# Optimization experiments

Hardware: AMD Instinct MI355X
Metric: run time of the kernel (lower is better)

Reference implementation:

```python
import jax, jax.numpy as jnp
import numpy as np

N_NODES = 20000
N_ATTRS = 5000
IN_FEATURES = 512
OUT_FEATURES = 128
ALPHA = 0.2  # LeakyReLU negative slope
NEG_INF = -9e15


def setup_inputs() -> dict:
    key = jax.random.key(0)
    k1, k2, k3, k4, k5 = jax.random.split(key, 5)
    node_embedding = jax.random.normal(k1, (N_NODES, IN_FEATURES), dtype=jnp.float32)
    attr_embedding = jax.random.normal(k2, (N_ATTRS, IN_FEATURES), dtype=jnp.float32)
    feat_mat = jax.random.randint(k3, (N_NODES, N_ATTRS), 0, 2, dtype=jnp.int32)
    # xavier_uniform with gain=1.414 (as in torch init)
    gain = 1.414
    lim_W = gain * np.sqrt(6.0 / (IN_FEATURES + OUT_FEATURES))
    W = jax.random.uniform(k4, (IN_FEATURES, OUT_FEATURES), minval=-lim_W, maxval=lim_W, dtype=jnp.float32)
    lim_a = gain * np.sqrt(6.0 / (2 * OUT_FEATURES + 1))
    a = jax.random.uniform(k5, (2 * OUT_FEATURES, 1), minval=-lim_a, maxval=lim_a, dtype=jnp.float32)
    return {"node_embedding": node_embedding, "attr_embedding": attr_embedding,
            "feat_mat": feat_mat, "W": W, "a": a}


def reference(node_embedding, attr_embedding, feat_mat, W, a):
    # Linear projections
    node_h = node_embedding @ W            # [N, F]
    attr_h = attr_embedding @ W            # [M, F]
    # Additive attention scores: e[i,j] = leakyrelu(a1.node_h[i] + a2.attr_h[j])
    wh1 = node_h @ a[:OUT_FEATURES, :]     # [N, 1]
    wh2 = attr_h @ a[OUT_FEATURES:, :]     # [M, 1]
    e = jax.nn.leaky_relu(wh1 + wh2.T, negative_slope=ALPHA)  # [N, M]
    # Mask where there is no node-attribute link, then softmax over attrs
    attention = jnp.where(feat_mat > 0, e, NEG_INF)
    attention = jax.nn.softmax(attention, axis=1)
    # (dropout is identity in eval mode)
    h_prime = attention @ attr_h           # [N, F]
    return jax.nn.elu(h_prime)             # concat=True branch
```

## Files before the change

### kernel.cpp

```cpp
#include <hip/hip_runtime.h>

#define N_NODES 20000
#define N_ATTRS 5000
#define IN_F    512
#define OUT_F   128
#define NK      160
#define NSS     80
#define WH2_PAD 5376
#define NEGBIG  -1e30f
#define LOG2E   1.4426950408889634f

typedef _Float16 f16x8 __attribute__((ext_vector_type(8)));
typedef float    f32x4 __attribute__((ext_vector_type(4)));
typedef int      i32x4 __attribute__((ext_vector_type(4)));

__device__ __forceinline__ float fast_exp2(float x) {
    return __builtin_amdgcn_exp2f(x);
}

__device__ __forceinline__ void async16(void* lds_dst, const void* gsrc) {
    __builtin_amdgcn_global_load_lds(
        (const __attribute__((address_space(1))) unsigned int*)gsrc,
        (__attribute__((address_space(3))) unsigned int*)lds_dst, 16, 0, 0);
}

__global__ __launch_bounds__(256) void prep_kernel(
    const float* __restrict__ W, const float* __restrict__ a,
    float* __restrict__ Wa1, float* __restrict__ Wa2, _Float16* __restrict__ Wp) {
    int gt = blockIdx.x * blockDim.x + threadIdx.x;
    if (gt < IN_F) {
        int k = gt;
        float s1 = 0.f, s2 = 0.f;
        for (int f = 0; f < OUT_F; ++f) {
            float w = W[k * OUT_F + f];
            s1 += w * a[f];
            s2 += w * a[OUT_F + f];
        }
        Wa1[k] = s1 * LOG2E;
        Wa2[k] = s2 * LOG2E;
    }
    for (int idx = gt; idx < IN_F * OUT_F; idx += gridDim.x * blockDim.x) {
        int j    = idx & 7;
        int lane = (idx >> 3) & 63;
        int nb   = (idx >> 9) & 7;
        int kb   = idx >> 12;
        int k = kb * 32 + (lane >> 4) * 8 + j;
        int n = nb * 16 + (lane & 15);
        Wp[idx] = (_Float16)W[k * OUT_F + n];
    }
}

__global__ __launch_bounds__(256) void wh_kernel(
    const float* __restrict__ node_emb, const float* __restrict__ attr_emb,
    const float* __restrict__ Wa1, const float* __restrict__ Wa2,
    float* __restrict__ wh1, float* __restrict__ wh2) {
    int wave = threadIdx.x >> 6, lane = threadIdx.x & 63;
    int r = blockIdx.x * 4 + wave;
    const float* src;
    const float* vec;
    float* dst;
    if (r < N_NODES) {
        src = node_emb + (size_t)r * IN_F; vec = Wa1; dst = wh1 + r;
    } else {
        int r2 = r - N_NODES;
        src = attr_emb + (size_t)r2 * IN_F; vec = Wa2; dst = wh2 + r2;
    }
    float4 ra = *reinterpret_cast<const float4*>(src + lane * 8);
    float4 rb = *reinterpret_cast<const float4*>(src + lane * 8 + 4);
    const float* vp = vec + lane * 8;
    float s = ra.x * vp[0] + ra.y * vp[1] + ra.z * vp[2] + ra.w * vp[3]
            + rb.x * vp[4] + rb.y * vp[5] + rb.z * vp[6] + rb.w * vp[7];
#pragma unroll
    for (int off = 1; off < 64; off <<= 1) s += __shfl_xor(s, off, 64);
    if (lane == 0) *dst = s;
}

__global__ __launch_bounds__(256) void max_kernel(
    float* __restrict__ wh2, float* __restrict__ maxp) {
    __shared__ float red[4];
    int t = threadIdx.x;
    float m = -1e30f;
    for (int j = t; j < N_ATTRS; j += 256) m = fmaxf(m, wh2[j]);
    for (int j = N_ATTRS + t; j < WH2_PAD; j += 256) wh2[j] = NEGBIG;
#pragma unroll
    for (int off = 1; off < 64; off <<= 1) m = fmaxf(m, __shfl_xor(m, off, 64));
    int wave = t >> 6, lane = t & 63;
    if (lane == 0) red[wave] = m;
    __syncthreads();
    if (t == 0) *maxp = fmaxf(fmaxf(red[0], red[1]), fmaxf(red[2], red[3]));
}

__global__ __launch_bounds__(64) void attr_h_kernel(
    const float* __restrict__ attr_emb, const _Float16* __restrict__ Wp,
    _Float16* __restrict__ Vp) {
    int lane = threadIdx.x & 63;
    int m = lane & 15, quad = lane >> 4;
    int j0 = blockIdx.x * 16;
    int j = j0 + m;
    bool valid = j < N_ATTRS;
    f32x4 acc[8];
#pragma unroll
    for (int nb = 0; nb < 8; ++nb)
#pragma unroll
        for (int t = 0; t < 4; ++t) acc[nb][t] = 0.f;
    const float* arow = attr_emb + (size_t)j * IN_F;
    for (int kk = 0; kk < IN_F / 32; ++kk) {
        f16x8 afrag;
        if (valid) {
            float4 ra = *reinterpret_cast<const float4*>(arow + kk * 32 + quad * 8);
            float4 rb = *reinterpret_cast<const float4*>(arow + kk * 32 + quad * 8 + 4);
            afrag[0] = (_Float16)ra.x; afrag[1] = (_Float16)ra.y;
            afrag[2] = (_Float16)ra.z; afrag[3] = (_Float16)ra.w;
            afrag[4] = (_Float16)rb.x; afrag[5] = (_Float16)rb.y;
            afrag[6] = (_Float16)rb.z; afrag[7] = (_Float16)rb.w;
        } else {
#pragma unroll
            for (int t = 0; t < 8; ++t) afrag[t] = (_Float16)0.f;
        }
        const _Float16* wbase = Wp + (size_t)(kk * 8) * 64 * 8;
#pragma unroll
        for (int nb = 0; nb < 8; ++nb) {
            f16x8 bfrag;
            __builtin_memcpy(&bfrag, wbase + (nb * 64 + lane) * 8, 16);
            acc[nb] = __builtin_amdgcn_mfma_f32_16x16x32_f16(afrag, bfrag, acc[nb], 0, 0, 0);
        }
    }
#pragma unroll
    for (int nb = 0; nb < 8; ++nb) {
#pragma unroll
        for (int reg = 0; reg < 4; ++reg) {
            int jr = j0 + quad * 4 + reg;
            int n = nb * 16 + m;
            float v = (jr < N_ATTRS) ? acc[nb][reg] : 0.f;
            size_t idx = ((size_t)((jr >> 5) * 8 + nb) * 64 +
                          (((jr >> 3) & 3) * 16 + m)) * 8 + (jr & 7);
            Vp[idx] = (_Float16)v;
        }
    }
}

__global__ __launch_bounds__(256) void pack_kernel(
    const int* __restrict__ feat, unsigned* __restrict__ fmask) {
    int u = blockIdx.x * 256 + threadIdx.x;
    int row = u / 160;
    int kk  = u - row * 160;
    int ko  = (kk & ~31) | ((kk & 31) ^ ((2 * (row & 15)) & 31));
    unsigned bits = 0;
    if (ko < 156) {
        const int* p = feat + (size_t)row * N_ATTRS + ko * 32;
#pragma unroll
        for (int q = 0; q < 8; ++q) {
            i32x4 v = *reinterpret_cast<const i32x4*>(p + q * 4);
            unsigned b = (v.x > 0 ? 1u : 0u) | (v.y > 0 ? 2u : 0u)
                       | (v.z > 0 ? 4u : 0u) | (v.w > 0 ? 8u : 0u);
            bits |= b << (q * 4);
        }
    } else if (ko == 156) {
        const int* p = feat + (size_t)row * N_ATTRS + 4992;
#pragma unroll
        for (int q = 0; q < 2; ++q) {
            i32x4 v = *reinterpret_cast<const i32x4*>(p + q * 4);
            unsigned b = (v.x > 0 ? 1u : 0u) | (v.y > 0 ? 2u : 0u)
                       | (v.z > 0 ? 4u : 0u) | (v.w > 0 ? 8u : 0u);
            bits |= b << (q * 4);
        }
    }
    fmask[u] = bits;
}

__global__ __launch_bounds__(256, 2) void attn_kernel(
    const unsigned* __restrict__ fmask, const float* __restrict__ wh1,
    const float* __restrict__ wh2, const float* __restrict__ maxwh2,
    const _Float16* __restrict__ Vp, float* __restrict__ out) {
    __shared__ __align__(16) char lds[20480];
    __shared__ float rsums[32];

    int wave = threadIdx.x >> 6, lane = threadIdx.x & 63;
    int m = lane & 15, quad = lane >> 4;
    int i0 = blockIdx.x * 32;
    int rg = (wave >> 1) * 16;
    int half = wave & 1;

    {
        const char* src = (const char*)(fmask + (size_t)i0 * 160);
#pragma unroll
        for (int q = 0; q < 5; ++q) {
            int off = q * 4096 + wave * 1024;
            async16(lds + off, src + off + lane * 16);
        }
    }

    float wh1i = wh1[i0 + rg + m];
    float emax = wh1i + maxwh2[0];
    float Mi = fmaxf(emax, 0.2f * emax) - 12.f;

    f32x4 acc[8];
#pragma unroll
    for (int nb = 0; nb < 8; ++nb)
#pragma unroll
        for (int t = 0; t < 4; ++t) acc[nb][t] = 0.f;
    float s = 0.f;

    const unsigned* fml = (const unsigned*)lds;
    int swz = (2 * m) & 31;
    int fbase = (rg + m) * 160;

    f16x8  bf0[8], bf1[8];
    float4 w0a, w0b, w1a, w1b;
    auto loadV = [&](int ss, f16x8* bf, float4& wa, float4& wb) {
        const _Float16* vb = Vp + (size_t)(2 * ss + half) * 4096 + lane * 8;
#pragma unroll
        for (int nb = 0; nb < 8; ++nb)
            bf[nb] = *reinterpret_cast<const f16x8*>(vb + nb * 512);
        const float* wp = wh2 + ss * 64 + half * 32 + quad * 8;
        wa = *reinterpret_cast<const float4*>(wp);
        wb = *reinterpret_cast<const float4*>(wp + 4);
    };

    auto compute = [&](int ss, const f16x8* bf, float4 wa, float4 wb) {
        int k = 2 * ss + half;
        int kk = (k & ~31) | ((k & 31) ^ swz);
        unsigned fm = fml[fbase + kk] >> (quad * 8);
        float wv[8] = {wa.x, wa.y, wa.z, wa.w, wb.x, wb.y, wb.z, wb.w};
        f16x8 afrag;
#pragma unroll
        for (int t = 0; t < 8; ++t) {
            float e = wh1i + wv[t];
            float l = fmaxf(e, 0.2f * e);
            float p = fast_exp2(l - Mi);
            p = (fm & (1u << t)) ? p : 0.f;
            _Float16 ph = (_Float16)p;
            s += (float)ph;
            afrag[t] = ph;
        }
#pragma unroll
        for (int nb = 0; nb < 8; ++nb)
            acc[nb] = __builtin_amdgcn_mfma_f32_16x16x32_f16(afrag, bf[nb], acc[nb], 0, 0, 0);
    };

    loadV(0, bf0, w0a, w0b);
    __syncthreads();

    for (int ss = 0; ss < NSS; ss += 2) {
        loadV(ss + 1, bf1, w1a, w1b);
        compute(ss, bf0, w0a, w0b);
        int kn = (ss + 2 < NSS) ? ss + 2 : NSS - 1;
        loadV(kn, bf0, w0a, w0b);
        compute(ss + 1, bf1, w1a, w1b);
    }

    s += __shfl_xor(s, 16, 64);
    s += __shfl_xor(s, 32, 64);

    __syncthreads();

    float* accp = (float*)lds;
    if (half == 0) {
#pragma unroll
        for (int nb = 0; nb < 8; ++nb)
#pragma unroll
            for (int reg = 0; reg < 4; ++reg)
                accp[(rg + quad * 4 + reg) * 128 + nb * 16 + m] = acc[nb][reg];
        if (lane < 16) rsums[rg + lane] = s;
    }
    __syncthreads();
    if (half == 1) {
#pragma unroll
        for (int nb = 0; nb < 8; ++nb)
#pragma unroll
            for (int reg = 0; reg < 4; ++reg)
                accp[(rg + quad * 4 + reg) * 128 + nb * 16 + m] += acc[nb][reg];
        if (lane < 16) rsums[rg + lane] += s;
    }
    __syncthreads();

    for (int o = threadIdx.x; o < 32 * 128; o += 256) {
        int lr = o >> 7, n = o & 127;
        float v = accp[lr * 128 + n];
        float rs = rsums[lr];
        rs = (rs > 0.f) ? rs : 1.f;
        float h = v / rs;
        float ov = (h > 0.f) ? h : (fast_exp2(h * LOG2E) - 1.f);
        out[(size_t)(i0 + lr) * OUT_F + n] = ov;
    }
}

extern "C" void kernel_launch(void* const* d_in, const int* in_sizes, int n_in,
                              void* d_out, int out_size, void* d_ws, size_t ws_size,
                              hipStream_t stream) {
    const float* node_emb = (const float*)d_in[0];
    const float* attr_emb = (const float*)d_in[1];
    const int*   feat     = (const int*)d_in[2];
    const float* W        = (const float*)d_in[3];
    const float* a        = (const float*)d_in[4];
    float*       out      = (float*)d_out;

    char* ws = (char*)d_ws;
    float*    Wa1 = (float*)(ws + 0);
    float*    Wa2 = (float*)(ws + 4096);
    float*    wh1 = (float*)(ws + 8192);
    float*    wh2 = (float*)(ws + 90112);
    float*    mx  = (float*)(ws + 111616);
    _Float16* Wp  = (_Float16*)(ws + 131072);
    _Float16* Vp  = (_Float16*)(ws + 262144);
    unsigned* fmk = (unsigned*)(ws + 2097152);

    prep_kernel<<<64, 256, 0, stream>>>(W, a, Wa1, Wa2, Wp);
    wh_kernel<<<6250, 256, 0, stream>>>(node_emb, attr_emb, Wa1, Wa2, wh1, wh2);
    max_kernel<<<1, 256, 0, stream>>>(wh2, mx);
    attr_h_kernel<<<320, 64, 0, stream>>>(attr_emb, Wp, Vp);
    pack_kernel<<<12500, 256, 0, stream>>>(feat, fmk);
    attn_kernel<<<625, 256, 0, stream>>>(fmk, wh1, wh2, mx, Vp, out);
}
```

Baseline: 671.7 us.

## Fuse pack, wh and attr_h kernels; restructure attention to 2 waves per block

Merges the mask packing, wh projection and attr_h MFMA kernels into one launch that dispatches on block index, so fewer kernel launches and tail gaps remain. The attention kernel now uses 128 threads where each wave handles 32 rows (two accumulator sets) and reads mask words directly from global memory rather than staging them into LDS with swizzling. This reuses each loaded V fragment for two row groups, but doubles the accumulator register footprint and halves the threads per block.

```diff
diff --git a/kernel.cpp b/kernel.cpp
--- a/kernel.cpp
+++ b/kernel.cpp
@@ -10,18 +10,16 @@
 #define NEGBIG  -1e30f
 #define LOG2E   1.4426950408889634f
 
+#define PACK_BLOCKS 12500
+#define WH_BLOCKS   6250
+#define AH_BLOCKS   80
+
 typedef _Float16 f16x8 __attribute__((ext_vector_type(8)));
 typedef float    f32x4 __attribute__((ext_vector_type(4)));
 typedef int      i32x4 __attribute__((ext_vector_type(4)));
 
 __device__ __forceinline__ float fast_exp2(float x) {
     return __builtin_amdgcn_exp2f(x);
-}
-
-__device__ __forceinline__ void async16(void* lds_dst, const void* gsrc) {
-    __builtin_amdgcn_global_load_lds(
-        (const __attribute__((address_space(1))) unsigned int*)gsrc,
-        (__attribute__((address_space(3))) unsigned int*)lds_dst, 16, 0, 0);
 }
 
 __global__ __launch_bounds__(256) void prep_kernel(
@@ -50,29 +48,103 @@
     }
 }
 
-__global__ __launch_bounds__(256) void wh_kernel(
+__global__ __launch_bounds__(256) void mega_kernel(
+    const int* __restrict__ feat, unsigned* __restrict__ fmask,
     const float* __restrict__ node_emb, const float* __restrict__ attr_emb,
     const float* __restrict__ Wa1, const float* __restrict__ Wa2,
-    float* __restrict__ wh1, float* __restrict__ wh2) {
+    float* __restrict__ wh1, float* __restrict__ wh2,
+    const _Float16* __restrict__ Wp, _Float16* __restrict__ Vp) {
+    int bid = blockIdx.x;
     int wave = threadIdx.x >> 6, lane = threadIdx.x & 63;
-    int r = blockIdx.x * 4 + wave;
-    const float* src;
-    const float* vec;
-    float* dst;
-    if (r < N_NODES) {
-        src = node_emb + (size_t)r * IN_F; vec = Wa1; dst = wh1 + r;
+
+    if (bid < PACK_BLOCKS) {
+        int u = bid * 256 + threadIdx.x;
+        int row = u / 160;
+        int k   = u - row * 160;
+        unsigned bits = 0;
+        if (k < 156) {
+            const int* p = feat + (size_t)row * N_ATTRS + k * 32;
+#pragma unroll
+            for (int q = 0; q < 8; ++q) {
+                i32x4 v = *reinterpret_cast<const i32x4*>(p + q * 4);
+                unsigned b = (v.x > 0 ? 1u : 0u) | (v.y > 0 ? 2u : 0u)
+                           | (v.z > 0 ? 4u : 0u) | (v.w > 0 ? 8u : 0u);
+                bits |= b << (q * 4);
+            }
+        } else if (k == 156) {
+            const int* p = feat + (size_t)row * N_ATTRS + 4992;
+#pragma unroll
+            for (int q = 0; q < 2; ++q) {
+                i32x4 v = *reinterpret_cast<const i32x4*>(p + q * 4);
+                unsigned b = (v.x > 0 ? 1u : 0u) | (v.y > 0 ? 2u : 0u)
+                           | (v.z > 0 ? 4u : 0u) | (v.w > 0 ? 8u : 0u);
+                bits |= b << (q * 4);
+            }
+        }
+        fmask[u] = bits;
+    } else if (bid < PACK_BLOCKS + WH_BLOCKS) {
+        int r = (bid - PACK_BLOCKS) * 4 + wave;
+        const float* src;
+        const float* vec;
+        float* dst;
+        if (r < N_NODES) {
+            src = node_emb + (size_t)r * IN_F; vec = Wa1; dst = wh1 + r;
+        } else {
+            int r2 = r - N_NODES;
+            src = attr_emb + (size_t)r2 * IN_F; vec = Wa2; dst = wh2 + r2;
+        }
+        float4 ra = *reinterpret_cast<const float4*>(src + lane * 8);
+        float4 rb = *reinterpret_cast<const float4*>(src + lane * 8 + 4);
+        const float* vp = vec + lane * 8;
+        float s = ra.x * vp[0] + ra.y * vp[1] + ra.z * vp[2] + ra.w * vp[3]
+                + rb.x * vp[4] + rb.y * vp[5] + rb.z * vp[6] + rb.w * vp[7];
+#pragma unroll
+        for (int off = 1; off < 64; off <<= 1) s += __shfl_xor(s, off, 64);
+        if (lane == 0) *dst = s;
     } else {
-        int r2 = r - N_NODES;
-        src = attr_emb + (size_t)r2 * IN_F; vec = Wa2; dst = wh2 + r2;
-    }
-    float4 ra = *reinterpret_cast<const float4*>(src + lane * 8);
-    float4 rb = *reinterpret_cast<const float4*>(src + lane * 8 + 4);
-    const float* vp = vec + lane * 8;
-    float s = ra.x * vp[0] + ra.y * vp[1] + ra.z * vp[2] + ra.w * vp[3]
-            + rb.x * vp[4] + rb.y * vp[5] + rb.z * vp[6] + rb.w * vp[7];
-#pragma unroll
-    for (int off = 1; off < 64; off <<= 1) s += __shfl_xor(s, off, 64);
-    if (lane == 0) *dst = s;
+        int m = lane & 15, quad = lane >> 4;
+        int j0 = ((bid - PACK_BLOCKS - WH_BLOCKS) * 4 + wave) * 16;
+        int j = j0 + m;
+        bool valid = j < N_ATTRS;
+        f32x4 acc[8];
+#pragma unroll
+        for (int nb = 0; nb < 8; ++nb)
+#pragma unroll
+            for (int t = 0; t < 4; ++t) acc[nb][t] = 0.f;
+        const float* arow = attr_emb + (size_t)j * IN_F;
+        for (int kk = 0; kk < IN_F / 32; ++kk) {
+            f16x8 afrag;
+            if (valid) {
+                float4 ra = *reinterpret_cast<const float4*>(arow + kk * 32 + quad * 8);
+                float4 rb = *reinterpret_cast<const float4*>(arow + kk * 32 + quad * 8 + 4);
+                afrag[0] = (_Float16)ra.x; afrag[1] = (_Float16)ra.y;
+                afrag[2] = (_Float16)ra.z; afrag[3] = (_Float16)ra.w;
+                afrag[4] = (_Float16)rb.x; afrag[5] = (_Float16)rb.y;
+                afrag[6] = (_Float16)rb.z; afrag[7] = (_Float16)rb.w;
+            } else {
+#pragma unroll
+                for (int t = 0; t < 8; ++t) afrag[t] = (_Float16)0.f;
+            }
+            const _Float16* wbase = Wp + (size_t)(kk * 8) * 64 * 8;
+#pragma unroll
+            for (int nb = 0; nb < 8; ++nb) {
+                f16x8 bfrag;
+                __builtin_memcpy(&bfrag, wbase + (nb * 64 + lane) * 8, 16);
+                acc[nb] = __builtin_amdgcn_mfma_f32_16x16x32_f16(afrag, bfrag, acc[nb], 0, 0, 0);
+            }
+        }
+#pragma unroll
+        for (int nb = 0; nb < 8; ++nb) {
+#pragma unroll
+            for (int reg = 0; reg < 4; ++reg) {
+                int jr = j0 + quad * 4 + reg;
+                float v = (jr < N_ATTRS) ? acc[nb][reg] : 0.f;
+                size_t idx = ((size_t)((jr >> 5) * 8 + nb) * 64 +
+                              (((jr >> 3) & 3) * 16 + m)) * 8 + (jr & 7);
+                Vp[idx] = (_Float16)v;
+            }
+        }
+    }
 }
 
 __global__ __launch_bounds__(256) void max_kernel(
@@ -90,191 +162,123 @@
     if (t == 0) *maxp = fmaxf(fmaxf(red[0], red[1]), fmaxf(red[2], red[3]));
 }
 
-__global__ __launch_bounds__(64) void attr_h_kernel(
-    const float* __restrict__ attr_emb, const _Float16* __restrict__ Wp,
-    _Float16* __restrict__ Vp) {
-    int lane = threadIdx.x & 63;
-    int m = lane & 15, quad = lane >> 4;
-    int j0 = blockIdx.x * 16;
-    int j = j0 + m;
-    bool valid = j < N_ATTRS;
-    f32x4 acc[8];
-#pragma unroll
-    for (int nb = 0; nb < 8; ++nb)
-#pragma unroll
-        for (int t = 0; t < 4; ++t) acc[nb][t] = 0.f;
-    const float* arow = attr_emb + (size_t)j * IN_F;
-    for (int kk = 0; kk < IN_F / 32; ++kk) {
-        f16x8 afrag;
-        if (valid) {
-            float4 ra = *reinterpret_cast<const float4*>(arow + kk * 32 + quad * 8);
-            float4 rb = *reinterpret_cast<const float4*>(arow + kk * 32 + quad * 8 + 4);
-            afrag[0] = (_Float16)ra.x; afrag[1] = (_Float16)ra.y;
-            afrag[2] = (_Float16)ra.z; afrag[3] = (_Float16)ra.w;
-            afrag[4] = (_Float16)rb.x; afrag[5] = (_Float16)rb.y;
-            afrag[6] = (_Float16)rb.z; afrag[7] = (_Float16)rb.w;
-        } else {
-#pragma unroll
-            for (int t = 0; t < 8; ++t) afrag[t] = (_Float16)0.f;
-        }
-        const _Float16* wbase = Wp + (size_t)(kk * 8) * 64 * 8;
-#pragma unroll
-        for (int nb = 0; nb < 8; ++nb) {
-            f16x8 bfrag;
-            __builtin_memcpy(&bfrag, wbase + (nb * 64 + lane) * 8, 16);
-            acc[nb] = __builtin_amdgcn_mfma_f32_16x16x32_f16(afrag, bfrag, acc[nb], 0, 0, 0);
-        }
-    }
-#pragma unroll
-    for (int nb = 0; nb < 8; ++nb) {
-#pragma unroll
-        for (int reg = 0; reg < 4; ++reg) {
-            int jr = j0 + quad * 4 + reg;
-            int n = nb * 16 + m;
-            float v = (jr < N_ATTRS) ? acc[nb][reg] : 0.f;
-            size_t idx = ((size_t)((jr >> 5) * 8 + nb) * 64 +
-                          (((jr >> 3) & 3) * 16 + m)) * 8 + (jr & 7);
-            Vp[idx] = (_Float16)v;
-        }
-    }
-}
-
-__global__ __launch_bounds__(256) void pack_kernel(
-    const int* __restrict__ feat, unsigned* __restrict__ fmask) {
-    int u = blockIdx.x * 256 + threadIdx.x;
-    int row = u / 160;
-    int kk  = u - row * 160;
-    int ko  = (kk & ~31) | ((kk & 31) ^ ((2 * (row & 15)) & 31));
-    unsigned bits = 0;
-    if (ko < 156) {
-        const int* p = feat + (size_t)row * N_ATTRS + ko * 32;
-#pragma unroll
-        for (int q = 0; q < 8; ++q) {
-            i32x4 v = *reinterpret_cast<const i32x4*>(p + q * 4);
-            unsigned b = (v.x > 0 ? 1u : 0u) | (v.y > 0 ? 2u : 0u)
-                       | (v.z > 0 ? 4u : 0u) | (v.w > 0 ? 8u : 0u);
-            bits |= b << (q * 4);
-        }
-    } else if (ko == 156) {
-        const int* p = feat + (size_t)row * N_ATTRS + 4992;
-#pragma unroll
-        for (int q = 0; q < 2; ++q) {
-            i32x4 v = *reinterpret_cast<const i32x4*>(p + q * 4);
-            unsigned b = (v.x > 0 ? 1u : 0u) | (v.y > 0 ? 2u : 0u)
-                       | (v.z > 0 ? 4u : 0u) | (v.w > 0 ? 8u : 0u);
-            bits |= b << (q * 4);
-        }
-    }
-    fmask[u] = bits;
-}
-
-__global__ __launch_bounds__(256, 2) void attn_kernel(
+__global__ __launch_bounds__(128) void attn_kernel(
     const unsigned* __restrict__ fmask, const float* __restrict__ wh1,
     const float* __restrict__ wh2, const float* __restrict__ maxwh2,
     const _Float16* __restrict__ Vp, float* __restrict__ out) {
-    __shared__ __align__(16) char lds[20480];
+    __shared__ float accp[32 * 128];
     __shared__ float rsums[32];
 
     int wave = threadIdx.x >> 6, lane = threadIdx.x & 63;
     int m = lane & 15, quad = lane >> 4;
     int i0 = blockIdx.x * 32;
-    int rg = (wave >> 1) * 16;
-    int half = wave & 1;
-
-    {
-        const char* src = (const char*)(fmask + (size_t)i0 * 160);
-#pragma unroll
-        for (int q = 0; q < 5; ++q) {
-            int off = q * 4096 + wave * 1024;
-            async16(lds + off, src + off + lane * 16);
-        }
-    }
-
-    float wh1i = wh1[i0 + rg + m];
-    float emax = wh1i + maxwh2[0];
-    float Mi = fmaxf(emax, 0.2f * emax) - 12.f;
-
-    f32x4 acc[8];
+    int half = wave;
+
+    float wh1a = wh1[i0 + m];
+    float wh1b = wh1[i0 + 16 + m];
+    float mx = maxwh2[0];
+    float ea = wh1a + mx, eb = wh1b + mx;
+    float Mia = fmaxf(ea, 0.2f * ea) - 12.f;
+    float Mib = fmaxf(eb, 0.2f * eb) - 12.f;
+
+    f32x4 acc[8], acc2[8];
 #pragma unroll
     for (int nb = 0; nb < 8; ++nb)
 #pragma unroll
-        for (int t = 0; t < 4; ++t) acc[nb][t] = 0.f;
-    float s = 0.f;
-
-    const unsigned* fml = (const unsigned*)lds;
-    int swz = (2 * m) & 31;
-    int fbase = (rg + m) * 160;
+        for (int t = 0; t < 4; ++t) { acc[nb][t] = 0.f; acc2[nb][t] = 0.f; }
+    float s = 0.f, s2 = 0.f;
+
+    const unsigned* f1p = fmask + (size_t)(i0 + m) * NK;
+    const unsigned* f2p = fmask + (size_t)(i0 + 16 + m) * NK;
 
     f16x8  bf0[8], bf1[8];
     float4 w0a, w0b, w1a, w1b;
-    auto loadV = [&](int ss, f16x8* bf, float4& wa, float4& wb) {
-        const _Float16* vb = Vp + (size_t)(2 * ss + half) * 4096 + lane * 8;
+    unsigned f1_0, f2_0, f1_1, f2_1;
+
+    auto loadSS = [&](int ss, f16x8* bf, float4& wa, float4& wb,
+                      unsigned& f1, unsigned& f2) {
+        int k = 2 * ss + half;
+        const _Float16* vb = Vp + (size_t)k * 4096 + lane * 8;
 #pragma unroll
         for (int nb = 0; nb < 8; ++nb)
             bf[nb] = *reinterpret_cast<const f16x8*>(vb + nb * 512);
-        const float* wp = wh2 + ss * 64 + half * 32 + quad * 8;
+        const float* wp = wh2 + k * 32 + quad * 8;
         wa = *reinterpret_cast<const float4*>(wp);
         wb = *reinterpret_cast<const float4*>(wp + 4);
+        f1 = f1p[k];
+        f2 = f2p[k];
     };
 
-    auto compute = [&](int ss, const f16x8* bf, float4 wa, float4 wb) {
-        int k = 2 * ss + half;
-        int kk = (k & ~31) | ((k & 31) ^ swz);
-        unsigned fm = fml[fbase + kk] >> (quad * 8);
+    auto computeSS = [&](const f16x8* bf, float4 wa, float4 wb,
+                         unsigned f1, unsigned f2) {
+        unsigned fm1 = f1 >> (quad * 8);
+        unsigned fm2 = f2 >> (quad * 8);
         float wv[8] = {wa.x, wa.y, wa.z, wa.w, wb.x, wb.y, wb.z, wb.w};
-        f16x8 afrag;
+        f16x8 a1, a2;
 #pragma unroll
         for (int t = 0; t < 8; ++t) {
-            float e = wh1i + wv[t];
-            float l = fmaxf(e, 0.2f * e);
-            float p = fast_exp2(l - Mi);
-            p = (fm & (1u << t)) ? p : 0.f;
-            _Float16 ph = (_Float16)p;
-            s += (float)ph;
-            afrag[t] = ph;
-        }
-#pragma unroll
-        for (int nb = 0; nb < 8; ++nb)
-            acc[nb] = __builtin_amdgcn_mfma_f32_16x16x32_f16(afrag, bf[nb], acc[nb], 0, 0, 0);
+            float e1 = wh1a + wv[t];
+            float l1 = fmaxf(e1, 0.2f * e1);
+            float p1 = fast_exp2(l1 - Mia);
+            p1 = (fm1 & (1u << t)) ? p1 : 0.f;
+            _Float16 ph1 = (_Float16)p1;
+            s += (float)ph1;
+            a1[t] = ph1;
+            float e2 = wh1b + wv[t];
+            float l2 = fmaxf(e2, 0.2f * e2);
+            float p2 = fast_exp2(l2 - Mib);
+            p2 = (fm2 & (1u << t)) ? p2 : 0.f;
+            _Float16 ph2 = (_Float16)p2;
+            s2 += (float)ph2;
+            a2[t] = ph2;
+        }
+#pragma unroll
+        for (int nb = 0; nb < 8; ++nb)
+            acc[nb] = __builtin_amdgcn_mfma_f32_16x16x32_f16(a1, bf[nb], acc[nb], 0, 0, 0);
+#pragma unroll
+        for (int nb = 0; nb < 8; ++nb)
+            acc2[nb] = __builtin_amdgcn_mfma_f32_16x16x32_f16(a2, bf[nb], acc2[nb], 0, 0, 0);
     };
 
-    loadV(0, bf0, w0a, w0b);
-    __syncthreads();
+    loadSS(0, bf0, w0a, w0b, f1_0, f2_0);
 
     for (int ss = 0; ss < NSS; ss += 2) {
-        loadV(ss + 1, bf1, w1a, w1b);
-        compute(ss, bf0, w0a, w0b);
+        loadSS(ss + 1, bf1, w1a, w1b, f1_1, f2_1);
+        computeSS(bf0, w0a, w0b, f1_0, f2_0);
         int kn = (ss + 2 < NSS) ? ss + 2 : NSS - 1;
-        loadV(kn, bf0, w0a, w0b);
-        compute(ss + 1, bf1, w1a, w1b);
+        loadSS(kn, bf0, w0a, w0b, f1_0, f2_0);
+        computeSS(bf1, w1a, w1b, f1_1, f2_1);
     }
 
     s += __shfl_xor(s, 16, 64);
     s += __shfl_xor(s, 32, 64);
-
+    s2 += __shfl_xor(s2, 16, 64);
+    s2 += __shfl_xor(s2, 32, 64);
+
+    if (wave == 0) {
+#pragma unroll
+        for (int nb = 0; nb < 8; ++nb)
+#pragma unroll
+            for (int reg = 0; reg < 4; ++reg) {
+                accp[(quad * 4 + reg) * 128 + nb * 16 + m] = acc[nb][reg];
+                accp[(16 + quad * 4 + reg) * 128 + nb * 16 + m] = acc2[nb][reg];
+            }
+        if (lane < 16) { rsums[m] = s; rsums[16 + m] = s2; }
+    }
     __syncthreads();
-
-    float* accp = (float*)lds;
-    if (half == 0) {
-#pragma unroll
-        for (int nb = 0; nb < 8; ++nb)
-#pragma unroll
-            for (int reg = 0; reg < 4; ++reg)
-                accp[(rg + quad * 4 + reg) * 128 + nb * 16 + m] = acc[nb][reg];
-        if (lane < 16) rsums[rg + lane] = s;
+    if (wave == 1) {
+#pragma unroll
+        for (int nb = 0; nb < 8; ++nb)
+#pragma unroll
+            for (int reg = 0; reg < 4; ++reg) {
+                accp[(quad * 4 + reg) * 128 + nb * 16 + m] += acc[nb][reg];
+                accp[(16 + quad * 4 + reg) * 128 + nb * 16 + m] += acc2[nb][reg];
+            }
+        if (lane < 16) { rsums[m] += s; rsums[16 + m] += s2; }
     }
     __syncthreads();
-    if (half == 1) {
-#pragma unroll
-        for (int nb = 0; nb < 8; ++nb)
-#pragma unroll
-            for (int reg = 0; reg < 4; ++reg)
-                accp[(rg + quad * 4 + reg) * 128 + nb * 16 + m] += acc[nb][reg];
-        if (lane < 16) rsums[rg + lane] += s;
-    }
-    __syncthreads();
-
-    for (int o = threadIdx.x; o < 32 * 128; o += 256) {
+
+    for (int o = threadIdx.x; o < 32 * 128; o += 128) {
         int lr = o >> 7, n = o & 127;
         float v = accp[lr * 128 + n];
         float rs = rsums[lr];
@@ -306,9 +310,8 @@
     unsigned* fmk = (unsigned*)(ws + 2097152);
 
     prep_kernel<<<64, 256, 0, stream>>>(W, a, Wa1, Wa2, Wp);
-    wh_kernel<<<6250, 256, 0, stream>>>(node_emb, attr_emb, Wa1, Wa2, wh1, wh2);
+    mega_kernel<<<PACK_BLOCKS + WH_BLOCKS + AH_BLOCKS, 256, 0, stream>>>(
+        feat, fmk, node_emb, attr_emb, Wa1, Wa2, wh1, wh2, Wp, Vp);
     max_kernel<<<1, 256, 0, stream>>>(wh2, mx);
-    attr_h_kernel<<<320, 64, 0, stream>>>(attr_emb, Wp, Vp);
-    pack_kernel<<<12500, 256, 0, stream>>>(feat, fmk);
-    attn_kernel<<<625, 256, 0, stream>>>(fmk, wh1, wh2, mx, Vp, out);
-}
+    attn_kernel<<<625, 128, 0, stream>>>(fmk, wh1, wh2, mx, Vp, out);
+}
```

After: 694.4 us. +3.4%, slower.
